# Optimization experiments

Hardware: AMD Instinct MI355X
Metric: run time of the kernel (lower is better)

Reference implementation:

```python
import jax, jax.numpy as jnp
import numpy as np

ALPHA = 2000.0   # alpha (bandwidth penalty)
K = 8            # number of modes
MAX_N = 20       # max ADMM iterations; tol=0 -> loop always runs MAX_N-1 iters
DC = False


def setup_inputs() -> dict:
    key = jax.random.key(0)
    signal = jax.random.normal(key, (16, 8192), dtype=jnp.float32)  # (C, T)
    return {"signal": signal}


def _forward(signal):
    C, T = signal.shape
    F = 2 * T
    # mirror extension -> (C, 2T)
    f = jnp.concatenate([signal[:, :T // 2][:, ::-1], signal, signal[:, T // 2:][:, ::-1]], axis=1)
    t = jnp.linspace(1.0 / F, 1.0, F)
    freqs = (t - 0.5 - 1.0 / F).astype(jnp.float32)                  # (F,)
    # NOTE: torch.fft.fftshift with default dim shifts ALL dims (incl. channel dim);
    # jnp.fft.fftshift with axes=None matches this behavior exactly.
    f_hat = jnp.fft.fftshift(jnp.fft.fft(f))
    f_hat_plus = f_hat.at[:, :F // 2].set(0)                         # zero negative freqs
    fpos = f_hat_plus.T.astype(jnp.complex64)                        # (F, C)
    freqs_c = freqs.astype(jnp.complex64)
    fh = freqs[F // 2:]                                              # positive freqs (F/2,)
    alpha_c = jnp.complex64(ALPHA)

    omega0 = ((0.5 / K) * jnp.arange(K, dtype=jnp.float32)).astype(jnp.complex64)  # init == 1
    u0 = jnp.zeros((F, K, C), jnp.complex64)
    sum0 = jnp.zeros((F, C), jnp.complex64)

    def omega_update(u_k):                                           # u_k: (F, C)
        p = jnp.abs(u_k[F // 2:, :]) ** 2                            # (F/2, C)
        return (jnp.sum(fh @ p) / jnp.sum(p)).astype(jnp.complex64)

    def step(carry, _):
        u_prev, omega_prev, sum_uk = carry
        sum_uk = sum_uk + u_prev[:, K - 1, :] - u_prev[:, 0, :]
        us, omegas = [], []
        for k in range(K):                                           # sequential mode recurrence
            if k > 0:
                sum_uk = sum_uk + us[k - 1] - u_prev[:, k, :]
            # torch uses omega from the PREVIOUS outer iteration for all modes
            denom = 1.0 + alpha_c * jnp.square(freqs_c - omega_prev[k])   # (F,)
            u_k = (fpos - sum_uk) / denom[:, None]   # lamda_hat stays 0 (never updated in torch)
            us.append(u_k)
            if k == 0 and DC:
                omegas.append(jnp.complex64(0.0))
            else:
                omegas.append(omega_update(u_k))
        u_curr = jnp.stack(us, axis=1)                               # (F, K, C)
        omega_curr = jnp.stack(omegas)                               # (K,)
        return (u_curr, omega_curr, sum_uk), omega_curr

    (u_fin, _, _), omega_hist = jax.lax.scan(step, (u0, omega0, sum0), None, length=MAX_N - 1)
    omega = jnp.concatenate([omega0[None, :], omega_hist], axis=0)   # (MAX_N, K)

    # Hermitian completion of the half-spectrum (matches torch index assignments & order)
    pos = u_fin[F // 2:, :, :]                                       # (F/2, K, C)
    u_hat = jnp.zeros((F, K, C), jnp.complex64)
    u_hat = u_hat.at[F // 2:].set(pos)
    u_hat = u_hat.at[jnp.arange(F // 2, 0, -1)].set(jnp.conj(pos))   # overwrites bin F/2 w/ conj
    u_hat = u_hat.at[0].set(jnp.conj(u_hat[-1]))

    u_time = jnp.fft.ifft(jnp.fft.ifftshift(u_hat, axes=0), axis=0).real  # (F, K, C)
    u_c = jnp.transpose(u_time, (1, 0, 2)).astype(jnp.complex64)          # (K, F, C)
    u_c = u_c[:, F // 4:3 * F // 4, :]                                    # crop mirror -> (K, T, C)
    u_hat2 = jnp.conj(jnp.fft.fftshift(jnp.fft.fft(u_c, axis=1), axes=1)) # (K, T, C)
    u_hat2 = jnp.transpose(u_hat2, (1, 0, 2))                             # (T, K, C)
    # torch applies ifftshift with dim=-1, which is the CHANNEL dim here; replicate faithfully
    u_out = jnp.fft.ifftshift(u_c, axes=-1).real                          # (K, T, C)
    return u_out, u_hat2, omega


def reference(signal):
    return _forward(signal)
```

## Files before the change

kernel.cpp:

```cpp
#include <hip/hip_runtime.h>
#include <math.h>

#define NPAIR 131072
#define STEPS 19
#define VMD_BLOCKS 256
#define ND_BANKS 16

#define SW(a) ((a) ^ (((a) >> 5) & 31))

#define LD_RLX(p)    __hip_atomic_load((p),       __ATOMIC_RELAXED, __HIP_MEMORY_SCOPE_AGENT)
#define ST_RLX(p,v)  __hip_atomic_store((p),(v),  __ATOMIC_RELAXED, __HIP_MEMORY_SCOPE_AGENT)
#define FAA_RLX(p,v) __hip_atomic_fetch_add((p),(v),__ATOMIC_RELAXED, __HIP_MEMORY_SCOPE_AGENT)

#define D_NDB   0
#define D_CNT   4864
#define D_OHIST 5400

__device__ __forceinline__ float2 cadd(float2 a, float2 b){ return make_float2(a.x+b.x, a.y+b.y); }
__device__ __forceinline__ float2 csub(float2 a, float2 b){ return make_float2(a.x-b.x, a.y-b.y); }
__device__ __forceinline__ float2 cmul(float2 a, float2 b){
    return make_float2(a.x*b.x - a.y*b.y, a.x*b.y + a.y*b.x);
}
template<int SGN>
__device__ __forceinline__ float2 imul(float2 a){
    return (SGN > 0) ? make_float2(-a.y, a.x) : make_float2(a.y, -a.x);
}

template<int SGN>
__device__ __forceinline__ void dft8(const float2* a, float2* y){
    const float C = 0.70710678118654752f;
    const float sg = (SGN > 0) ? 1.f : -1.f;
    float2 t0 = cadd(a[0], a[4]), t1 = csub(a[0], a[4]);
    float2 t2 = cadd(a[2], a[6]), t3 = imul<SGN>(csub(a[2], a[6]));
    float2 E0 = cadd(t0, t2), E2 = csub(t0, t2), E1 = cadd(t1, t3), E3 = csub(t1, t3);
    float2 s0 = cadd(a[1], a[5]), s1 = csub(a[1], a[5]);
    float2 s2 = cadd(a[3], a[7]), s3 = imul<SGN>(csub(a[3], a[7]));
    float2 O0 = cadd(s0, s2), O2 = csub(s0, s2), O1 = cadd(s1, s3), O3 = csub(s1, s3);
    float2 w1 = make_float2(C, sg * C), w3 = make_float2(-C, sg * C);
    float2 R0 = O0, R1 = cmul(O1, w1), R2 = imul<SGN>(O2), R3 = cmul(O3, w3);
    y[0] = cadd(E0, R0); y[4] = csub(E0, R0);
    y[1] = cadd(E1, R1); y[5] = csub(E1, R1);
    y[2] = cadd(E2, R2); y[6] = csub(E2, R2);
    y[3] = cadd(E3, R3); y[7] = csub(E3, R3);
}

template<int SGN>
__device__ void lds_fft8192_r8(float2* lds, int tid){
    #pragma unroll
    for (int pi = 0; pi < 4; pi++){
        int ls = 3 * pi;
        int s  = 1 << ls;
        int nn = 8192 >> ls;
        int q = tid & (s - 1);
        float2 a[8], y[8];
        #pragma unroll
        for (int r = 0; r < 8; r++) a[r] = lds[SW(tid + (r << 10))];
        __syncthreads();
        dft8<SGN>(a, y);
        int p = tid >> ls;
        float ang = (float)(2 * p) / (float)nn;
        float sn, cs;
        sincospif(SGN > 0 ? ang : -ang, &sn, &cs);
        float2 w = make_float2(cs, sn);
        float2 wk = make_float2(1.f, 0.f);
        int o = q + ((tid - q) << 3);
        lds[SW(o)] = y[0];
        #pragma unroll
        for (int k = 1; k < 8; k++){
            wk = cmul(wk, w);
            lds[SW(o + (k << ls))] = cmul(y[k], wk);
        }
        __syncthreads();
    }
    #pragma unroll
    for (int w4 = 0; w4 < 4; w4++){
        int idx = (w4 << 10) + tid;
        float2 a = lds[SW(idx)], b = lds[SW(idx + 4096)];
        lds[SW(idx)]        = cadd(a, b);
        lds[SW(idx + 4096)] = csub(a, b);
    }
    __syncthreads();
}

template<int SGN>
__device__ void lds_fft4096_r8(float2* lds, int tid){
    #pragma unroll
    for (int pi = 0; pi < 4; pi++){
        int ls = 3 * pi;
        int s  = 1 << ls;
        int nn = 4096 >> ls;
        float2 a[8], y[8];
        int q = tid & (s - 1);
        if (tid < 512){
            #pragma unroll
            for (int r = 0; r < 8; r++) a[r] = lds[SW(tid + (r << 9))];
        }
        __syncthreads();
        if (tid < 512){
            dft8<SGN>(a, y);
            int p = tid >> ls;
            float ang = (float)(2 * p) / (float)nn;
            float sn, cs;
            sincospif(SGN > 0 ? ang : -ang, &sn, &cs);
            float2 w = make_float2(cs, sn);
            float2 wk = make_float2(1.f, 0.f);
            int o = q + ((tid - q) << 3);
            lds[SW(o)] = y[0];
            #pragma unroll
            for (int k = 1; k < 8; k++){
                wk = cmul(wk, w);
                lds[SW(o + (k << ls))] = cmul(y[k], wk);
            }
        }
        __syncthreads();
    }
}

__global__ __launch_bounds__(512) void k_stageA(const float* __restrict__ sig,
                                                float2* __restrict__ C,
                                                double* __restrict__ D){
    extern __shared__ float2 lds[];
    int tid = threadIdx.x;
    int bb  = blockIdx.x;
    int zi = bb * 512 + tid;
    if (zi < 5400) D[zi] = 0.0;
    int cw = bb >> 2, r4 = bb & 3;
    int cs = (cw + 8) & 15;
    const float* sp = sig + cs * 8192;
    #pragma unroll
    for (int i = 0; i < 8; i++){
        int p = i * 512 + tid;
        int x = 4 * p + r4;
        int mx = (x < 4096) ? (4095 - x) : ((x < 12288) ? (x - 4096) : (20479 - x));
        lds[SW(p)] = make_float2(sp[mx], 0.f);
    }
    __syncthreads();
    lds_fft4096_r8<-1>(lds, tid);
    float2* dst = C + (size_t)bb * 4096;
    #pragma unroll
    for (int i = 0; i < 8; i++){
        int j = i * 512 + tid;
        dst[j] = lds[SW(j)];
    }
}

__global__ __launch_bounds__(512, 2) void k_vmd_all(const float2* __restrict__ C,
                                                    float2* __restrict__ U,
                                                    double* __restrict__ D){
    double* NDB   = D + D_NDB;
    int*    CNT   = (int*)(D + D_CNT);
    double* OHIST = D + D_OHIST;

    int tid = blockIdx.x * 512 + threadIdx.x;
    int j = tid & 8191;
    int cw = tid >> 13;
    float fr = (float)j / 16384.0f;
    const float2* Cb = C + (size_t)(cw * 4) * 4096;
    int m = j & 4095;
    float2 C0 = Cb[m], C1 = Cb[4096 + m], C2 = Cb[8192 + m], C3 = Cb[12288 + m];
    float s1, c1, s2, c2;
    sincospif(-(float)j / 8192.0f, &s1, &c1);
    sincospif(-(float)j / 4096.0f, &s2, &c2);
    float2 w1 = make_float2(c1, s1), w2 = make_float2(c2, s2), w3 = cmul(w1, w2);
    float2 fv = cadd(cadd(C0, cmul(w1, C1)), cadd(cmul(w2, C2), cmul(w3, C3)));
    float fx = fv.x, fy = fv.y;
    float urx[8], ury[8], om[8];
    #pragma unroll
    for (int k = 0; k < 8; k++){ urx[k] = 0.f; ury[k] = 0.f; om[k] = 0.0625f * (float)k; }
    __shared__ float  lred[8][16];
    __shared__ double ndls[256];
    __shared__ double om_s[8];
    int lane = threadIdx.x & 63, wv = threadIdx.x >> 6;
    int mybank = (blockIdx.x & (ND_BANKS - 1)) * 16;
    int grp = blockIdx.x >> 4;

    for (int step = 0; step < STEPS; step++){
        if (step > 0){
            #pragma unroll
            for (int k = 0; k < 8; k++) om[k] = (float)om_s[k];
        }
        float sx = 0.f, sy = 0.f;
        #pragma unroll
        for (int k = 1; k < 8; k++){ sx += urx[k]; sy += ury[k]; }
        float lx = 0.f, ly = 0.f, nloc[8], dloc[8];
        #pragma unroll
        for (int k = 0; k < 8; k++){
            if (k > 0){ sx += lx - urx[k]; sy += ly - ury[k]; }
            float d = fr - om[k];
            float den = 1.0f + 2000.0f * d * d;
            float rden = 1.0f / den;
            float nx = (fx - sx) * rden, ny = (fy - sy) * rden;
            urx[k] = nx; ury[k] = ny;
            lx = nx; ly = ny;
            float pw = nx * nx + ny * ny;
            nloc[k] = fr * pw; dloc[k] = pw;
        }
        float s8[8];
        {
            bool hi = (lane & 32) != 0;
            #pragma unroll
            for (int k = 0; k < 8; k++){
                float t = hi ? nloc[k] : dloc[k];
                float r = __shfl_xor(t, 32);
                s8[k] = (hi ? dloc[k] : nloc[k]) + r;
            }
        }
        float s4v[4];
        {
            bool hi = (lane & 16) != 0;
            #pragma unroll
            for (int k = 0; k < 4; k++){
                float t = hi ? s8[k] : s8[k + 4];
                float r = __shfl_xor(t, 16);
                s4v[k] = (hi ? s8[k + 4] : s8[k]) + r;
            }
        }
        float s2v[2];
        {
            bool hi = (lane & 8) != 0;
            #pragma unroll
            for (int k = 0; k < 2; k++){
                float t = hi ? s4v[k] : s4v[k + 2];
                float r = __shfl_xor(t, 8);
                s2v[k] = (hi ? s4v[k + 2] : s4v[k]) + r;
            }
        }
        float sv;
        {
            bool hi = (lane & 4) != 0;
            float t = hi ? s2v[0] : s2v[1];
            float r = __shfl_xor(t, 4);
            sv = (hi ? s2v[1] : s2v[0]) + r;
        }
        sv += __shfl_xor(sv, 2);
        sv += __shfl_xor(sv, 1);
        if ((lane & 3) == 0) lred[wv][lane >> 2] = sv;
        __syncthreads();
        if (threadIdx.x < 16){
            double sum = 0.0;
            #pragma unroll
            for (int w = 0; w < 8; w++) sum += (double)lred[w][threadIdx.x];
            atomicAdd(&NDB[step * 256 + mybank + threadIdx.x], sum);
        }
        __syncthreads();
        if (step < STEPS - 1){
            if (threadIdx.x == 0){
                int target = 16 * (step + 1);
                int old = FAA_RLX(&CNT[grp * 32], 1);
                bool released = false;
                if (old == target - 1){
                    int rold = FAA_RLX(&CNT[512], 1);
                    if (rold == target - 1){
                        #pragma unroll
                        for (int g = 0; g < 16; g++)
                            ST_RLX(&CNT[576 + g * 32], step + 1);
                        released = true;
                    }
                }
                if (!released)
                    while (LD_RLX(&CNT[576 + grp * 32]) <= step)
                        __builtin_amdgcn_s_sleep(1);
            }
            __syncthreads();
            if (threadIdx.x < 256)
                ndls[threadIdx.x] = LD_RLX(&NDB[step * 256 + threadIdx.x]);
            __syncthreads();
            if (threadIdx.x < 8){
                double n_ = 0.0, d_ = 0.0;
                #pragma unroll
                for (int bk = 0; bk < ND_BANKS; bk++){
                    n_ += ndls[bk * 16 + threadIdx.x];
                    d_ += ndls[bk * 16 + 8 + threadIdx.x];
                }
                double v = n_ / d_;
                om_s[threadIdx.x] = v;
                if (blockIdx.x == 0)
                    ST_RLX(&OHIST[step * 8 + threadIdx.x], v);
            }
            __syncthreads();
        }
    }
    #pragma unroll
    for (int k = 0; k < 8; k++) U[k * NPAIR + tid] = make_float2(urx[k], ury[k]);
}

__global__ __launch_bounds__(1024) void k_stageCD(float2* __restrict__ U){
    extern __shared__ float2 lds[];
    int tid = threadIdx.x;
    int b = blockIdx.x;
    const float2* pos = U + b * 8192;
    float* slice = (float*)(U) + (size_t)b * 16384;
    const float inv = 1.0f / 16384.0f;
    #pragma unroll
    for (int r = 0; r < 8; r++){
        int p = r * 1024 + tid;
        float2 Hk, HkM;
        if (p == 0){
            Hk  = make_float2(pos[0].x, 0.f);
            HkM = make_float2(pos[8191].x, 0.f);
        } else {
            Hk = pos[p];
            float2 q2 = pos[8192 - p];
            HkM = make_float2(q2.x, -q2.y);
        }
        float2 S  = cadd(Hk, HkM);
        float2 Dv = csub(Hk, HkM);
        float sn, cn;
        sincospif((float)p / 8192.0f, &sn, &cn);
        float2 c = cmul(make_float2(cn, sn), Dv);
        lds[SW(p)] = make_float2(S.x - c.y, S.y + c.x);
    }
    __syncthreads();
    lds_fft8192_r8<1>(lds, tid);
    float2 zreg[4];
    #pragma unroll
    for (int q = 2; q < 6; q++){
        int n = q * 1024 + tid;
        float2 z = lds[SW(n)];
        zreg[q - 2] = make_float2(z.x * inv, z.y * inv);
        *(float2*)&slice[2 * n - 4096] = zreg[q - 2];
    }
    __syncthreads();
    #pragma unroll
    for (int q = 0; q < 4; q++)
        lds[SW(q * 1024 + tid)] = zreg[q];
    __syncthreads();
    lds_fft4096_r8<-1>(lds, tid);
    #pragma unroll
    for (int q = 0; q < 4; q++){
        int k = q * 1024 + tid;
        float2 Wk = lds[SW(k)];
        float2 Wm = lds[SW((4096 - k) & 4095)];
        float ax = 0.5f * (Wk.x + Wm.x);
        float dx = Wk.x - Wm.x, dy = Wk.y + Wm.y;
        float bx = 0.5f * dy, by = -0.5f * dx;
        float sn, cn;
        sincospif(-(float)k / 4096.0f, &sn, &cn);
        float rey = ax + cn * bx - sn * by;
        slice[12288 + k] = rey;
        if (k > 0) slice[12288 - k] = rey;
        else       slice[8192]      = Wk.x - Wk.y;
    }
}

__global__ __launch_bounds__(256) void k_outs(const float* __restrict__ U32,
                                              const double* __restrict__ Dbase,
                                              float* __restrict__ out){
    __shared__ double smemd[128 * 65 / 2 + 140];
    float* smem = (float*)smemd;
    int bx = blockIdx.x;
    int tid = threadIdx.x;
    if (bx < 256){
        float (*tile)[257] = (float(*)[257])smem;
        int k  = bx >> 5;
        int t0 = (bx & 31) * 256;
        #pragma unroll
        for (int cw = 0; cw < 16; cw++)
            tile[cw][tid] = U32[((size_t)(k * 16 + cw)) * 16384 + t0 + tid];
        __syncthreads();
        #pragma unroll
        for (int i = 0; i < 16; i++){
            int flat = i * 256 + tid;
            int dt = flat >> 4, ch = flat & 15;
            int cw = (ch + 8) & 15;
            out[(size_t)k * 131072 + t0 * 16 + flat] = tile[cw][dt];
        }
    } else if (bx < 384){
        float (*tile)[65] = (float(*)[65])smem;
        int t0 = (bx - 256) * 64;
        #pragma unroll
        for (int i = 0; i < 32; i++){
            int flat = i * 256 + tid;
            int b = flat >> 6, dt = flat & 63;
            tile[b][dt] = U32[(size_t)b * 16384 + 8192 + t0 + dt];
        }
        __syncthreads();
        #pragma unroll
        for (int i = 0; i < 32; i++){
            int flat = i * 256 + tid;
            int dt = flat >> 7, b = flat & 127;
            out[1048576 + (size_t)(t0 + dt) * 128 + b] = tile[b][dt];
        }
    } else {
        const double* NDB   = Dbase + D_NDB;
        const double* OHIST = Dbase + D_OHIST;
        double* dsm = smemd;
        if (tid < 256) dsm[tid] = NDB[18 * 256 + tid];
        __syncthreads();
        if (tid < 8){
            double n_ = 0.0, d_ = 0.0;
            #pragma unroll
            for (int bk = 0; bk < ND_BANKS; bk++){
                n_ += dsm[bk * 16 + tid];
                d_ += dsm[bk * 16 + 8 + tid];
            }
            dsm[256 + tid] = n_ / d_;
        }
        __syncthreads();
        if (tid < 160){
            int row = tid >> 3, k = tid & 7;
            double v;
            if (row == 0)       v = 0.0625 * (double)k;
            else if (row <= 18) v = OHIST[(row - 1) * 8 + k];
            else                v = dsm[256 + k];
            out[2097152 + tid] = (float)v;
        }
    }
}

extern "C" void kernel_launch(void* const* d_in, const int* in_sizes, int n_in,
                              void* d_out, int out_size, void* d_ws, size_t ws_size,
                              hipStream_t stream){
    const float* sig = (const float*)d_in[0];
    float* out = (float*)d_out;
    char* p = (char*)d_ws;
    float2* U = (float2*)p;
    float2* C = (float2*)p;
    double* D = (double*)(p + (size_t)8 * 1024 * 1024);

    k_stageA<<<dim3(64), dim3(512), 32768, stream>>>(sig, C, D);
    k_vmd_all<<<dim3(VMD_BLOCKS), dim3(512), 0, stream>>>(C, U, D);
    k_stageCD<<<dim3(128), dim3(1024), 65536, stream>>>(U);
    k_outs<<<dim3(385), dim3(256), 0, stream>>>((const float*)U, D, out);
}
```

Measured before the change: 151.4 us.

## Fuse stage-A FFT into persistent VMD kernel behind a grid barrier

The separate stage-A FFT kernel is folded into the persistent VMD kernel. The first 64 blocks compute the mirrored-signal FFTs and store them with relaxed atomics, and a software grid barrier then makes them visible before all blocks read C. The zeroing of the reduction/counter area moves to a hipMemsetAsync, so one kernel launch is replaced by a memset. In exchange, the VMD kernel now needs 32 KB of dynamic LDS, which may lower occupancy, and it pays for one extra grid barrier round while most blocks sit idle during the FFT phase.

```diff
diff --git a/kernel.cpp b/kernel.cpp
--- a/kernel.cpp
+++ b/kernel.cpp
@@ -116,48 +116,70 @@
     }
 }
 
-__global__ __launch_bounds__(512) void k_stageA(const float* __restrict__ sig,
-                                                float2* __restrict__ C,
-                                                double* __restrict__ D){
-    extern __shared__ float2 lds[];
-    int tid = threadIdx.x;
-    int bb  = blockIdx.x;
-    int zi = bb * 512 + tid;
-    if (zi < 5400) D[zi] = 0.0;
-    int cw = bb >> 2, r4 = bb & 3;
-    int cs = (cw + 8) & 15;
-    const float* sp = sig + cs * 8192;
-    #pragma unroll
-    for (int i = 0; i < 8; i++){
-        int p = i * 512 + tid;
-        int x = 4 * p + r4;
-        int mx = (x < 4096) ? (4095 - x) : ((x < 12288) ? (x - 4096) : (20479 - x));
-        lds[SW(p)] = make_float2(sp[mx], 0.f);
-    }
-    __syncthreads();
-    lds_fft4096_r8<-1>(lds, tid);
-    float2* dst = C + (size_t)bb * 4096;
-    #pragma unroll
-    for (int i = 0; i < 8; i++){
-        int j = i * 512 + tid;
-        dst[j] = lds[SW(j)];
-    }
-}
-
-__global__ __launch_bounds__(512, 2) void k_vmd_all(const float2* __restrict__ C,
+__device__ __forceinline__ void gbar(int* CNT, int grp, int round){
+    int target = 16 * round;
+    int old = FAA_RLX(&CNT[grp * 32], 1);
+    bool released = false;
+    if (old == target - 1){
+        int rold = FAA_RLX(&CNT[512], 1);
+        if (rold == target - 1){
+            #pragma unroll
+            for (int g = 0; g < 16; g++)
+                ST_RLX(&CNT[576 + g * 32], round);
+            released = true;
+        }
+    }
+    if (!released)
+        while (LD_RLX(&CNT[576 + grp * 32]) < round)
+            __builtin_amdgcn_s_sleep(1);
+}
+
+__global__ __launch_bounds__(512, 2) void k_vmd_all(const float* __restrict__ sig,
+                                                    float2* __restrict__ C,
                                                     float2* __restrict__ U,
                                                     double* __restrict__ D){
+    extern __shared__ float2 lds[];
     double* NDB   = D + D_NDB;
     int*    CNT   = (int*)(D + D_CNT);
     double* OHIST = D + D_OHIST;
 
     int tid = blockIdx.x * 512 + threadIdx.x;
+    int lane = threadIdx.x & 63, wv = threadIdx.x >> 6;
+    int mybank = (blockIdx.x & (ND_BANKS - 1)) * 16;
+    int grp = blockIdx.x >> 4;
+
+    if (blockIdx.x < 64){
+        int bb = blockIdx.x;
+        int cwa = bb >> 2, r4 = bb & 3;
+        int cs = (cwa + 8) & 15;
+        const float* sp = sig + cs * 8192;
+        #pragma unroll
+        for (int i = 0; i < 8; i++){
+            int p = i * 512 + threadIdx.x;
+            int x = 4 * p + r4;
+            int mx = (x < 4096) ? (4095 - x) : ((x < 12288) ? (x - 4096) : (20479 - x));
+            lds[SW(p)] = make_float2(sp[mx], 0.f);
+        }
+        __syncthreads();
+        lds_fft4096_r8<-1>(lds, threadIdx.x);
+        float2* dst = C + (size_t)bb * 4096;
+        #pragma unroll
+        for (int i = 0; i < 8; i++){
+            int j2 = i * 512 + threadIdx.x;
+            ST_RLX(&dst[j2], lds[SW(j2)]);
+        }
+    }
+    __syncthreads();
+    if (threadIdx.x == 0) gbar(CNT, grp, 1);
+    __syncthreads();
+
     int j = tid & 8191;
     int cw = tid >> 13;
     float fr = (float)j / 16384.0f;
     const float2* Cb = C + (size_t)(cw * 4) * 4096;
     int m = j & 4095;
-    float2 C0 = Cb[m], C1 = Cb[4096 + m], C2 = Cb[8192 + m], C3 = Cb[12288 + m];
+    float2 C0 = LD_RLX(&Cb[m]),        C1 = LD_RLX(&Cb[4096 + m]);
+    float2 C2 = LD_RLX(&Cb[8192 + m]), C3 = LD_RLX(&Cb[12288 + m]);
     float s1, c1, s2, c2;
     sincospif(-(float)j / 8192.0f, &s1, &c1);
     sincospif(-(float)j / 4096.0f, &s2, &c2);
@@ -170,9 +192,6 @@
     __shared__ float  lred[8][16];
     __shared__ double ndls[256];
     __shared__ double om_s[8];
-    int lane = threadIdx.x & 63, wv = threadIdx.x >> 6;
-    int mybank = (blockIdx.x & (ND_BANKS - 1)) * 16;
-    int grp = blockIdx.x >> 4;
 
     for (int step = 0; step < STEPS; step++){
         if (step > 0){
@@ -244,23 +263,7 @@
         }
         __syncthreads();
         if (step < STEPS - 1){
-            if (threadIdx.x == 0){
-                int target = 16 * (step + 1);
-                int old = FAA_RLX(&CNT[grp * 32], 1);
-                bool released = false;
-                if (old == target - 1){
-                    int rold = FAA_RLX(&CNT[512], 1);
-                    if (rold == target - 1){
-                        #pragma unroll
-                        for (int g = 0; g < 16; g++)
-                            ST_RLX(&CNT[576 + g * 32], step + 1);
-                        released = true;
-                    }
-                }
-                if (!released)
-                    while (LD_RLX(&CNT[576 + grp * 32]) <= step)
-                        __builtin_amdgcn_s_sleep(1);
-            }
+            if (threadIdx.x == 0) gbar(CNT, grp, step + 2);
             __syncthreads();
             if (threadIdx.x < 256)
                 ndls[threadIdx.x] = LD_RLX(&NDB[step * 256 + threadIdx.x]);
@@ -418,8 +421,8 @@
     float2* C = (float2*)p;
     double* D = (double*)(p + (size_t)8 * 1024 * 1024);
 
-    k_stageA<<<dim3(64), dim3(512), 32768, stream>>>(sig, C, D);
-    k_vmd_all<<<dim3(VMD_BLOCKS), dim3(512), 0, stream>>>(C, U, D);
+    hipMemsetAsync(D, 0, 5400 * sizeof(double), stream);
+    k_vmd_all<<<dim3(VMD_BLOCKS), dim3(512), 32768, stream>>>(sig, C, U, D);
     k_stageCD<<<dim3(128), dim3(1024), 65536, stream>>>(U);
     k_outs<<<dim3(385), dim3(256), 0, stream>>>((const float*)U, D, out);
 }
```

New measurement: 153.0 us. No clear change (+1.0%).
